# Performance work log

Hardware: AMD Instinct MI355X
Metric: run time of the kernel (lower is better)

The kernel has to match this reference:

```python
import jax, jax.numpy as jnp
import numpy as np

N, E, B = 100000, 1200000, 512
IN_DIM, HID, K, NCLS = 64, 64, 3, 10


def setup_inputs() -> dict:
    key = jax.random.key(0)
    ks = jax.random.split(key, 10)
    features = jax.random.normal(ks[0], (N, IN_DIM), jnp.float32)
    edge_src = jax.random.randint(ks[1], (E,), 0, N)
    edge_dst = jax.random.randint(ks[2], (E,), 0, N)
    graph_ids = jnp.sort(jax.random.randint(ks[3], (N,), 0, B))
    s1 = float(1.0 / np.sqrt(IN_DIM))
    W1 = jax.random.uniform(ks[4], (IN_DIM, HID), jnp.float32, -s1, s1)
    b1 = jnp.zeros((HID,), jnp.float32)
    s2 = float(1.0 / np.sqrt(HID))
    W2 = jax.random.uniform(ks[5], (HID, HID), jnp.float32, -s2, s2)
    b2 = jnp.zeros((HID,), jnp.float32)
    s3 = float(1.0 / np.sqrt(HID * 3))
    cw = jax.random.uniform(ks[6], (HID, HID, 3), jnp.float32, -s3, s3)
    cb = jax.random.uniform(ks[7], (HID,), jnp.float32, -s3, s3)
    Wc = jax.random.uniform(ks[8], (HID, NCLS), jnp.float32, -s2, s2)
    bc = jax.random.uniform(ks[9], (NCLS,), jnp.float32, -s2, s2)
    return dict(features=features, edge_src=edge_src, edge_dst=edge_dst,
                graph_ids=graph_ids, num_graphs=B,
                W1=W1, b1=b1, W2=W2, b2=b2, cw=cw, cb=cb, Wc=Wc, bc=bc)


def graph_conv(h, src, dst, W, b, n_nodes):
    # DGL GraphConv, norm='both', allow_zero_in_degree (degrees clamped to 1)
    ones = jnp.ones((src.shape[0],), h.dtype)
    out_deg = jnp.zeros((n_nodes,), h.dtype).at[src].add(ones)
    in_deg = jnp.zeros((n_nodes,), h.dtype).at[dst].add(ones)
    norm_s = jax.lax.rsqrt(jnp.clip(out_deg, 1.0, None))
    norm_d = jax.lax.rsqrt(jnp.clip(in_deg, 1.0, None))
    m = (h * norm_s[:, None]) @ W  # weight first; math identical to agg-first
    agg = jnp.zeros((n_nodes, W.shape[1]), h.dtype).at[dst].add(m[src])
    return agg * norm_d[:, None] + b


def sort_pool(h, gid, num_graphs, k):
    # DGL SortPooling: sort each node's features ascending along feature dim,
    # then take top-k nodes per graph by last feature value (descending),
    # zero-padding graphs with < k nodes. Output [num_graphs, k*D].
    hs = jnp.sort(h, axis=-1)
    key = hs[:, -1]
    order = jnp.lexsort((-key, gid))  # gid asc, key desc
    gid_s = gid[order]
    hs_s = hs[order]
    n = gid.shape[0]
    start = jnp.full((num_graphs,), n).at[gid_s].min(jnp.arange(n))
    rank = jnp.arange(n) - start[gid_s]  # within-graph rank by key desc
    mask = rank < k
    slot = gid_s * k + jnp.clip(rank, 0, k - 1)
    out = jnp.zeros((num_graphs * k, hs.shape[-1]), h.dtype).at[slot].add(
        jnp.where(mask[:, None], hs_s, jnp.zeros((), h.dtype)))
    return out.reshape(num_graphs, k * hs.shape[-1])


def reference(features, edge_src, edge_dst, graph_ids, num_graphs,
              W1, b1, W2, b2, cw, cb, Wc, bc):
    n = features.shape[0]
    h = jax.nn.relu(graph_conv(features, edge_src, edge_dst, W1, b1, n))
    h = jax.nn.relu(graph_conv(h, edge_src, edge_dst, W2, b2, n))
    p = sort_pool(h, graph_ids, num_graphs, K)          # [B, K*HID]
    x = p.reshape(num_graphs, HID, K)                    # faithful torch reshape
    # Conv1d(kernel=3, stride=1) on length-3 input -> length-1 output
    y = jax.nn.relu(jnp.einsum('bct,oct->bo', x, cw) + cb)
    return y @ Wc + bc
```

## Files before the change

kernel.cpp:

```cpp
#include <hip/hip_runtime.h>
#include <hip/hip_bf16.h>


#define PART 6272
#define HALFP (PART / 2)
#define MCH  64

__global__ void k_hist2(const int* __restrict__ esrc, const int* __restrict__ edst,
                        unsigned char* __restrict__ hd, unsigned char* __restrict__ hs,
                        int N, int E, int P) {
  __shared__ unsigned int ld[HALFP];
  __shared__ unsigned int ls[HALFP];
  const int b = blockIdx.x;
  const int p = b % P;
  const int m = b / P;
  const int base = p * PART;
  const int lim = min(PART, N - base);
  for (int i = threadIdx.x; i < HALFP; i += blockDim.x) { ld[i] = 0u; ls[i] = 0u; }
  __syncthreads();
  const long long cb = (long long)m * E / MCH;
  const long long ce = (long long)(m + 1) * E / MCH;
  const long long a0 = min((cb + 3) & ~3LL, ce);
  const long long nv = (ce - a0) >> 2;
  for (long long e = cb + threadIdx.x; e < a0; e += blockDim.x) {
    int d = edst[e] - base;
    if ((unsigned)d < (unsigned)lim) atomicAdd(&ld[d >> 1], 1u << ((d & 1) * 16));
    int s = esrc[e] - base;
    if ((unsigned)s < (unsigned)lim) atomicAdd(&ls[s >> 1], 1u << ((s & 1) * 16));
  }
  const int4* __restrict__ d4p = (const int4*)(edst + a0);
  const int4* __restrict__ s4p = (const int4*)(esrc + a0);
  for (long long i = threadIdx.x; i < nv; i += blockDim.x) {
    int4 d4 = d4p[i];
    int4 s4 = s4p[i];
    int d;
    d = d4.x - base; if ((unsigned)d < (unsigned)lim) atomicAdd(&ld[d >> 1], 1u << ((d & 1) * 16));
    d = d4.y - base; if ((unsigned)d < (unsigned)lim) atomicAdd(&ld[d >> 1], 1u << ((d & 1) * 16));
    d = d4.z - base; if ((unsigned)d < (unsigned)lim) atomicAdd(&ld[d >> 1], 1u << ((d & 1) * 16));
    d = d4.w - base; if ((unsigned)d < (unsigned)lim) atomicAdd(&ld[d >> 1], 1u << ((d & 1) * 16));
    d = s4.x - base; if ((unsigned)d < (unsigned)lim) atomicAdd(&ls[d >> 1], 1u << ((d & 1) * 16));
    d = s4.y - base; if ((unsigned)d < (unsigned)lim) atomicAdd(&ls[d >> 1], 1u << ((d & 1) * 16));
    d = s4.z - base; if ((unsigned)d < (unsigned)lim) atomicAdd(&ls[d >> 1], 1u << ((d & 1) * 16));
    d = s4.w - base; if ((unsigned)d < (unsigned)lim) atomicAdd(&ls[d >> 1], 1u << ((d & 1) * 16));
  }
  for (long long e = a0 + (nv << 2) + threadIdx.x; e < ce; e += blockDim.x) {
    int d = edst[e] - base;
    if ((unsigned)d < (unsigned)lim) atomicAdd(&ld[d >> 1], 1u << ((d & 1) * 16));
    int s = esrc[e] - base;
    if ((unsigned)s < (unsigned)lim) atomicAdd(&ls[s >> 1], 1u << ((s & 1) * 16));
  }
  __syncthreads();
  unsigned char* sd = hd + ((size_t)p * MCH + m) * PART;
  unsigned char* ss = hs + ((size_t)p * MCH + m) * PART;
  for (int i = threadIdx.x; i < lim; i += blockDim.x) {
    sd[i] = (unsigned char)((ld[i >> 1] >> ((i & 1) * 16)) & 0xffffu);
    ss[i] = (unsigned char)((ls[i >> 1] >> ((i & 1) * 16)) & 0xffffu);
  }
}

__global__ void k_off(unsigned char* __restrict__ hd, const unsigned char* __restrict__ hs,
                      int* __restrict__ deg_d, float* __restrict__ norm_s,
                      float* __restrict__ norm_d, int N, int P) {
  int v = blockIdx.x * blockDim.x + threadIdx.x;
  if (v >= N) return;
  int p = v / PART, loc = v % PART;
  size_t base = (size_t)p * MCH * PART + loc;
  int run = 0;
#pragma unroll
  for (int m = 0; m < MCH; ++m) {
    int t = hd[base + (size_t)m * PART];
    hd[base + (size_t)m * PART] = (unsigned char)run;
    run += t;
  }
  int s = 0;
#pragma unroll
  for (int m = 0; m < MCH; ++m) s += hs[base + (size_t)m * PART];
  deg_d[v] = run;
  norm_d[v] = rsqrtf((float)max(run, 1));
  norm_s[v] = rsqrtf((float)max(s, 1));
}

__global__ void k_scan1(const int* __restrict__ deg, int* __restrict__ rowptr,
                        int* __restrict__ bsum, int N) {
  __shared__ int sums[256];
  const int t = threadIdx.x;
  const int base = blockIdx.x * 2048 + t * 8;
  int loc[8];
  int tot = 0;
#pragma unroll
  for (int j = 0; j < 8; ++j) {
    int idx = base + j;
    loc[j] = tot;
    tot += (idx < N) ? deg[idx] : 0;
  }
  sums[t] = tot;
  __syncthreads();
  for (int off = 1; off < 256; off <<= 1) {
    int x = (t >= off) ? sums[t - off] : 0;
    __syncthreads();
    sums[t] += x;
    __syncthreads();
  }
  int excl = (t == 0) ? 0 : sums[t - 1];
#pragma unroll
  for (int j = 0; j < 8; ++j) {
    int idx = base + j;
    if (idx < N) rowptr[idx] = excl + loc[j];
  }
  if (t == 255) bsum[blockIdx.x] = sums[255];
}

__global__ void k_scan2(int* __restrict__ bsum, int nb) {
  int lane = threadIdx.x;
  int v = (lane < nb) ? bsum[lane] : 0;
  int inc = v;
#pragma unroll
  for (int off = 1; off < 64; off <<= 1) {
    int o = __shfl_up(inc, off, 64);
    if (lane >= off) inc += o;
  }
  if (lane < nb) bsum[lane] = inc - v;
}

__global__ void k_scan3(int* __restrict__ rowptr, const int* __restrict__ bsum, int N) {
  int v = blockIdx.x * blockDim.x + threadIdx.x;
  if (v < N) rowptr[v] += bsum[v >> 11];
}

__global__ void k_fill2(const int* __restrict__ esrc, const int* __restrict__ edst,
                        const unsigned char* __restrict__ hd, const int* __restrict__ rowptr,
                        int* __restrict__ csr, int N, int E, int P) {
  __shared__ int cur[PART];
  const int b = blockIdx.x;
  const int p = b % P;
  const int m = b / P;
  const int base = p * PART;
  const int lim = min(PART, N - base);
  const unsigned char* slice = hd + ((size_t)p * MCH + m) * PART;
  for (int i = threadIdx.x; i < lim; i += blockDim.x)
    cur[i] = rowptr[base + i] + (int)slice[i];
  __syncthreads();
  const long long cb = (long long)m * E / MCH;
  const long long ce = (long long)(m + 1) * E / MCH;
  const long long a0 = min((cb + 3) & ~3LL, ce);
  const long long nv = (ce - a0) >> 2;
  for (long long e = cb + threadIdx.x; e < a0; e += blockDim.x) {
    int d = edst[e] - base;
    if ((unsigned)d < (unsigned)lim) csr[atomicAdd(&cur[d], 1)] = esrc[e];
  }
  const int4* __restrict__ d4p = (const int4*)(edst + a0);
  const int4* __restrict__ s4p = (const int4*)(esrc + a0);
  for (long long i = threadIdx.x; i < nv; i += blockDim.x) {
    int4 d4 = d4p[i];
    int4 s4 = s4p[i];
    int d;
    d = d4.x - base; if ((unsigned)d < (unsigned)lim) csr[atomicAdd(&cur[d], 1)] = s4.x;
    d = d4.y - base; if ((unsigned)d < (unsigned)lim) csr[atomicAdd(&cur[d], 1)] = s4.y;
    d = d4.z - base; if ((unsigned)d < (unsigned)lim) csr[atomicAdd(&cur[d], 1)] = s4.z;
    d = d4.w - base; if ((unsigned)d < (unsigned)lim) csr[atomicAdd(&cur[d], 1)] = s4.w;
  }
  for (long long e = a0 + (nv << 2) + threadIdx.x; e < ce; e += blockDim.x) {
    int d = edst[e] - base;
    if ((unsigned)d < (unsigned)lim) csr[atomicAdd(&cur[d], 1)] = esrc[e];
  }
}

__global__ void __launch_bounds__(256) k_gemm64(
    const float* __restrict__ in, const float* __restrict__ norm,
    const float* __restrict__ W, float* __restrict__ out, int N) {
  __shared__ float Wl[4096];
  __shared__ float Ac[64 * 136];
  const int t = threadIdx.x;
  const int ch = (t & 7) * 8;
  const int nb = (t >> 3) * 4;
  for (int i = t; i < 1024; i += 256)
    ((float4*)Wl)[i] = ((const float4*)W)[i];

  const int NT = (N + 127) >> 7;
  for (int tile = blockIdx.x; tile < NT; tile += gridDim.x) {
    const int vbase = tile << 7;
    __syncthreads();
    for (int i = t; i < 2048; i += 256) {
      const int r = i >> 4;
      const int c = (i & 15) * 4;
      const int v = vbase + r;
      float4 val = make_float4(0.f, 0.f, 0.f, 0.f);
      if (v < N) val = *(const float4*)(in + (size_t)v * 64 + c);
      Ac[(c + 0) * 136 + r] = val.x;
      Ac[(c + 1) * 136 + r] = val.y;
      Ac[(c + 2) * 136 + r] = val.z;
      Ac[(c + 3) * 136 + r] = val.w;
    }
    __syncthreads();

    float acc[4][8];
#pragma unroll
    for (int j = 0; j < 4; ++j)
#pragma unroll
      for (int c = 0; c < 8; ++c) acc[j][c] = 0.f;

    for (int k = 0; k < 64; k += 4) {
#pragma unroll
      for (int kk = 0; kk < 4; ++kk) {
        const float4 aa = *(const float4*)&Ac[(k + kk) * 136 + nb];
        const float4 w0 = *(const float4*)&Wl[(k + kk) * 64 + ch];
        const float4 w1 = *(const float4*)&Wl[(k + kk) * 64 + ch + 4];
        const float an[4] = {aa.x, aa.y, aa.z, aa.w};
        const float wn[8] = {w0.x, w0.y, w0.z, w0.w, w1.x, w1.y, w1.z, w1.w};
#pragma unroll
        for (int j = 0; j < 4; ++j)
#pragma unroll
          for (int c = 0; c < 8; ++c)
            acc[j][c] = fmaf(an[j], wn[c], acc[j][c]);
      }
    }

#pragma unroll
    for (int j = 0; j < 4; ++j) {
      const int v = vbase + nb + j;
      if (v < N) {
        const float nm = norm[v];
        float4 o0, o1;
        o0.x = acc[j][0] * nm; o0.y = acc[j][1] * nm;
        o0.z = acc[j][2] * nm; o0.w = acc[j][3] * nm;
        o1.x = acc[j][4] * nm; o1.y = acc[j][5] * nm;
        o1.z = acc[j][6] * nm; o1.w = acc[j][7] * nm;
        *(float4*)(out + (size_t)v * 64 + ch)     = o0;
        *(float4*)(out + (size_t)v * 64 + ch + 4) = o1;
      }
    }
  }
}

__global__ void k_gather(const float* __restrict__ m, const int* __restrict__ rowptr,
                         const int* __restrict__ deg, const float* __restrict__ norm_d,
                         const float* __restrict__ bias, const int* __restrict__ csr,
                         float* __restrict__ h, float* __restrict__ key, int N) {
  const int w = blockIdx.x * (blockDim.x >> 6) + (threadIdx.x >> 6);
  if (w >= N) return;
  const int lane = threadIdx.x & 63;
  const int quad = lane & 15;
  const int grp = lane >> 4;
  const int start = rowptr[w];
  const int cnt = deg[w];
  float4 acc0 = make_float4(0.f, 0.f, 0.f, 0.f);
  float4 acc1 = make_float4(0.f, 0.f, 0.f, 0.f);
  int i = grp;
  for (; i + 4 < cnt; i += 8) {
    int s0 = csr[start + i];
    int s1 = csr[start + i + 4];
    const float4 v0 = *(const float4*)(m + (size_t)s0 * 64 + quad * 4);
    const float4 v1 = *(const float4*)(m + (size_t)s1 * 64 + quad * 4);
    acc0.x += v0.x; acc0.y += v0.y; acc0.z += v0.z; acc0.w += v0.w;
    acc1.x += v1.x; acc1.y += v1.y; acc1.z += v1.z; acc1.w += v1.w;
  }
  if (i < cnt) {
    int s0 = csr[start + i];
    const float4 v0 = *(const float4*)(m + (size_t)s0 * 64 + quad * 4);
    acc0.x += v0.x; acc0.y += v0.y; acc0.z += v0.z; acc0.w += v0.w;
  }
  acc0.x += acc1.x; acc0.y += acc1.y; acc0.z += acc1.z; acc0.w += acc1.w;
#pragma unroll
  for (int off = 16; off <= 32; off <<= 1) {
    acc0.x += __shfl_xor(acc0.x, off, 64);
    acc0.y += __shfl_xor(acc0.y, off, 64);
    acc0.z += __shfl_xor(acc0.z, off, 64);
    acc0.w += __shfl_xor(acc0.w, off, 64);
  }
  const float nd = norm_d[w];
  const float4 bq = *(const float4*)(bias + quad * 4);
  float4 o;
  o.x = fmaxf(fmaf(acc0.x, nd, bq.x), 0.f);
  o.y = fmaxf(fmaf(acc0.y, nd, bq.y), 0.f);
  o.z = fmaxf(fmaf(acc0.z, nd, bq.z), 0.f);
  o.w = fmaxf(fmaf(acc0.w, nd, bq.w), 0.f);
  if (grp == 0) *(float4*)(h + (size_t)w * 64 + quad * 4) = o;
  if (key != nullptr) {
    float mx = fmaxf(fmaxf(o.x, o.y), fmaxf(o.z, o.w));
#pragma unroll
    for (int off = 1; off < 16; off <<= 1) mx = fmaxf(mx, __shfl_xor(mx, off, 64));
    if (lane == 0) key[w] = mx;
  }
}

__global__ void k_bstart(const int* __restrict__ gid, int* __restrict__ gstart, int N) {
  int i = blockIdx.x * blockDim.x + threadIdx.x;
  if (i >= N) return;
  int g = gid[i];
  if (i == 0 || gid[i - 1] != g) gstart[g] = i;
}

__global__ void k_bfin(const int* __restrict__ gstart, int* __restrict__ gcnt,
                       int B, int N) {
  __shared__ int sm[512];
  const int g = threadIdx.x;
  sm[g] = (g < B) ? gstart[g] : 0x7fffffff;
  __syncthreads();
  for (int off = 1; off < 512; off <<= 1) {
    int x = (g + off < 512) ? sm[g + off] : 0x7fffffff;
    __syncthreads();
    sm[g] = min(sm[g], x);
    __syncthreads();
  }
  if (g < B) {
    int gs = gstart[g];
    int ns = (g + 1 < 512) ? min(sm[g + 1], N) : N;
    gcnt[g] = (gs < N) ? (ns - gs) : 0;
  }
}

__global__ void k_top3(const float* __restrict__ key, const int* __restrict__ gstart,
                       const int* __restrict__ gcnt, int* __restrict__ sel, int B) {
  const int lane = threadIdx.x & 63;
  const int g = blockIdx.x * (blockDim.x >> 6) + (threadIdx.x >> 6);
  if (g >= B) return;
  const int s = gstart[g], c = gcnt[g];
  float v0 = -1.f, v1 = -1.f, v2 = -1.f;
  int i0 = 0x7fffffff, i1 = 0x7fffffff, i2 = 0x7fffffff;
  for (int i = s + lane; i < s + c; i += 64) {
    float kv = key[i];
    if (kv > v0 || (kv == v0 && i < i0)) {
      v2 = v1; i2 = i1; v1 = v0; i1 = i0; v0 = kv; i0 = i;
    } else if (kv > v1 || (kv == v1 && i < i1)) {
      v2 = v1; i2 = i1; v1 = kv; i1 = i;
    } else if (kv > v2 || (kv == v2 && i < i2)) {
      v2 = kv; i2 = i;
    }
  }
  int ptr = 0;
  for (int r = 0; r < 3; ++r) {
    float mv = (ptr == 0) ? v0 : (ptr == 1) ? v1 : (ptr == 2) ? v2 : -1.f;
    int   mi = (ptr == 0) ? i0 : (ptr == 1) ? i1 : (ptr == 2) ? i2 : 0x7fffffff;
    float bv = mv; int bi = mi;
#pragma unroll
    for (int off = 32; off; off >>= 1) {
      float ov = __shfl_xor(bv, off, 64);
      int   oi = __shfl_xor(bi, off, 64);
      if (ov > bv || (ov == bv && oi < bi)) { bv = ov; bi = oi; }
    }
    if (bi == mi && ptr < 3) ptr++;
    if (lane == 0) sel[g * 3 + r] = (bi == 0x7fffffff) ? -1 : bi;
  }
}

__global__ void k_pool(const float* __restrict__ h, const int* __restrict__ sel,
                       float* __restrict__ p, int B) {
  const int lane = threadIdx.x & 63;
  const int w = blockIdx.x * (blockDim.x >> 6) + (threadIdx.x >> 6);
  if (w >= B * 3) return;
  int node = sel[w];
  float v = 0.f;
  if (node >= 0) {
    v = h[(size_t)node * 64 + lane];
    for (int k2 = 2; k2 <= 64; k2 <<= 1) {
      for (int j = k2 >> 1; j > 0; j >>= 1) {
        float o = __shfl_xor(v, j, 64);
        bool up = ((lane & k2) == 0);
        bool lower = ((lane & j) == 0);
        v = (lower == up) ? fminf(v, o) : fmaxf(v, o);
      }
    }
  }
  p[(size_t)w * 64 + lane] = v;
}

__global__ void k_cls(const float* __restrict__ p, const float* __restrict__ cw,
                      const float* __restrict__ cb, const float* __restrict__ Wc,
                      const float* __restrict__ bc, float* __restrict__ out, int B) {
  __shared__ float prow[192];
  const int b = blockIdx.x;
  const int lane = threadIdx.x;
  prow[lane] = p[(size_t)b * 192 + lane];
  prow[lane + 64] = p[(size_t)b * 192 + lane + 64];
  prow[lane + 128] = p[(size_t)b * 192 + lane + 128];
  __syncthreads();
  float y = cb[lane];
  for (int j = 0; j < 192; ++j) y = fmaf(prow[j], cw[lane * 192 + j], y);
  float ry = fmaxf(y, 0.f);
  for (int c = 0; c < 10; ++c) {
    float s = ry * Wc[lane * 10 + c];
#pragma unroll
    for (int off = 32; off; off >>= 1) s += __shfl_xor(s, off, 64);
    if (lane == 0) out[b * 10 + c] = s + bc[c];
  }
}

extern "C" void kernel_launch(void* const* d_in, const int* in_sizes, int n_in,
                              void* d_out, int out_size, void* d_ws, size_t ws_size,
                              hipStream_t stream) {
  const float* features = (const float*)d_in[0];
  const int*   esrc     = (const int*)d_in[1];
  const int*   edst     = (const int*)d_in[2];
  const int*   gid      = (const int*)d_in[3];
  const float* W1 = (const float*)d_in[5];
  const float* b1 = (const float*)d_in[6];
  const float* W2 = (const float*)d_in[7];
  const float* b2 = (const float*)d_in[8];
  const float* cw = (const float*)d_in[9];
  const float* cb = (const float*)d_in[10];
  const float* Wc = (const float*)d_in[11];
  const float* bc = (const float*)d_in[12];
  float* out = (float*)d_out;

  const int N = in_sizes[0] / 64;
  const int E = in_sizes[1];
  const int B = out_size / 10;
  const size_t N64 = (size_t)N * 64;
  const int nscan = (N + 2047) / 2048;
  const int P = (N + PART - 1) / PART;
  const size_t HSZ = (size_t)P * MCH * PART;
  const int NT = (N + 127) / 128;

  float* bufA   = (float*)d_ws;
  float* bufB   = bufA + N64;
  int*   deg_d  = (int*)(bufB + N64);
  float* norm_s = (float*)(deg_d + N);
  float* norm_d = norm_s + N;
  float* key    = norm_d + N;
  int*   rowptr = (int*)(key + N);
  int*   csr    = rowptr + N;
  int*   bsum   = csr + E;
  int*   gstart = bsum + 64;
  int*   gcnt   = gstart + B;
  int*   sel    = gcnt + B;
  float* p      = (float*)(sel + 3 * B);
  unsigned char* hd = (unsigned char*)(p + 192 * B);
  unsigned char* hs = hd + HSZ;

  const int TB = 256;

  k_hist2<<<P * MCH, TB, 0, stream>>>(esrc, edst, hd, hs, N, E, P);
  k_off<<<(N + TB - 1) / TB, TB, 0, stream>>>(hd, hs, deg_d, norm_s, norm_d, N, P);
  k_scan1<<<nscan, 256, 0, stream>>>(deg_d, rowptr, bsum, N);
  k_scan2<<<1, 64, 0, stream>>>(bsum, nscan);
  k_scan3<<<(N + TB - 1) / TB, TB, 0, stream>>>(rowptr, bsum, N);
  k_fill2<<<P * MCH, TB, 0, stream>>>(esrc, edst, hd, rowptr, csr, N, E, P);

  k_gemm64<<<NT, TB, 0, stream>>>(features, norm_s, W1, bufA, N);
  k_gather<<<(N + 3) / 4, TB, 0, stream>>>(bufA, rowptr, deg_d, norm_d, b1, csr,
                                           bufB, nullptr, N);

  k_gemm64<<<NT, TB, 0, stream>>>(bufB, norm_s, W2, bufA, N);
  k_gather<<<(N + 3) / 4, TB, 0, stream>>>(bufA, rowptr, deg_d, norm_d, b2, csr,
                                           bufB, key, N);

  hipMemsetAsync(gstart, 0x7f, (size_t)B * sizeof(int), stream);
  k_bstart<<<(N + TB - 1) / TB, TB, 0, stream>>>(gid, gstart, N);
  k_bfin<<<1, 512, 0, stream>>>(gstart, gcnt, B, N);
  k_top3<<<(B + 3) / 4, TB, 0, stream>>>(key, gstart, gcnt, sel, B);
  k_pool<<<(B * 3 + 3) / 4, TB, 0, stream>>>(bufB, sel, p, B);

  k_cls<<<B, 64, 0, stream>>>(p, cw, cb, Wc, bc, out, B);
}
```

Before: 322.9 us.

## Split histogram per array and pack fill cursors into byte counters

```diff
diff --git a/kernel.cpp b/kernel.cpp
--- a/kernel.cpp
+++ b/kernel.cpp
@@ -2,79 +2,71 @@
 #include <hip/hip_bf16.h>
 
 
-#define PART 6272
-#define HALFP (PART / 2)
+#define PART_H 25088
+#define HALF_H (PART_H / 2)
+#define PART_F 12544
+#define QUART_F (PART_F / 4)
 #define MCH  64
 
-__global__ void k_hist2(const int* __restrict__ esrc, const int* __restrict__ edst,
+__global__ void k_hist1(const int* __restrict__ esrc, const int* __restrict__ edst,
                         unsigned char* __restrict__ hd, unsigned char* __restrict__ hs,
-                        int N, int E, int P) {
-  __shared__ unsigned int ld[HALFP];
-  __shared__ unsigned int ls[HALFP];
+                        int N, int E, int PH) {
+  __shared__ unsigned int lc[HALF_H];
   const int b = blockIdx.x;
-  const int p = b % P;
-  const int m = b / P;
-  const int base = p * PART;
-  const int lim = min(PART, N - base);
-  for (int i = threadIdx.x; i < HALFP; i += blockDim.x) { ld[i] = 0u; ls[i] = 0u; }
+  const int half = PH * MCH;
+  const int a = b / half;
+  const int r = b % half;
+  const int p = r % PH;
+  const int m = r / PH;
+  const int* __restrict__ arr = a ? esrc : edst;
+  unsigned char* __restrict__ outp = a ? hs : hd;
+  const int base = p * PART_H;
+  const int lim = min(PART_H, N - base);
+  for (int i = threadIdx.x; i < HALF_H; i += blockDim.x) lc[i] = 0u;
   __syncthreads();
   const long long cb = (long long)m * E / MCH;
   const long long ce = (long long)(m + 1) * E / MCH;
   const long long a0 = min((cb + 3) & ~3LL, ce);
   const long long nv = (ce - a0) >> 2;
   for (long long e = cb + threadIdx.x; e < a0; e += blockDim.x) {
-    int d = edst[e] - base;
-    if ((unsigned)d < (unsigned)lim) atomicAdd(&ld[d >> 1], 1u << ((d & 1) * 16));
-    int s = esrc[e] - base;
-    if ((unsigned)s < (unsigned)lim) atomicAdd(&ls[s >> 1], 1u << ((s & 1) * 16));
-  }
-  const int4* __restrict__ d4p = (const int4*)(edst + a0);
-  const int4* __restrict__ s4p = (const int4*)(esrc + a0);
+    int d = arr[e] - base;
+    if ((unsigned)d < (unsigned)lim) atomicAdd(&lc[d >> 1], 1u << ((d & 1) * 16));
+  }
+  const int4* __restrict__ a4p = (const int4*)(arr + a0);
   for (long long i = threadIdx.x; i < nv; i += blockDim.x) {
-    int4 d4 = d4p[i];
-    int4 s4 = s4p[i];
+    int4 v4 = a4p[i];
     int d;
-    d = d4.x - base; if ((unsigned)d < (unsigned)lim) atomicAdd(&ld[d >> 1], 1u << ((d & 1) * 16));
-    d = d4.y - base; if ((unsigned)d < (unsigned)lim) atomicAdd(&ld[d >> 1], 1u << ((d & 1) * 16));
-    d = d4.z - base; if ((unsigned)d < (unsigned)lim) atomicAdd(&ld[d >> 1], 1u << ((d & 1) * 16));
-    d = d4.w - base; if ((unsigned)d < (unsigned)lim) atomicAdd(&ld[d >> 1], 1u << ((d & 1) * 16));
-    d = s4.x - base; if ((unsigned)d < (unsigned)lim) atomicAdd(&ls[d >> 1], 1u << ((d & 1) * 16));
-    d = s4.y - base; if ((unsigned)d < (unsigned)lim) atomicAdd(&ls[d >> 1], 1u << ((d & 1) * 16));
-    d = s4.z - base; if ((unsigned)d < (unsigned)lim) atomicAdd(&ls[d >> 1], 1u << ((d & 1) * 16));
-    d = s4.w - base; if ((unsigned)d < (unsigned)lim) atomicAdd(&ls[d >> 1], 1u << ((d & 1) * 16));
+    d = v4.x - base; if ((unsigned)d < (unsigned)lim) atomicAdd(&lc[d >> 1], 1u << ((d & 1) * 16));
+    d = v4.y - base; if ((unsigned)d < (unsigned)lim) atomicAdd(&lc[d >> 1], 1u << ((d & 1) * 16));
+    d = v4.z - base; if ((unsigned)d < (unsigned)lim) atomicAdd(&lc[d >> 1], 1u << ((d & 1) * 16));
+    d = v4.w - base; if ((unsigned)d < (unsigned)lim) atomicAdd(&lc[d >> 1], 1u << ((d & 1) * 16));
   }
   for (long long e = a0 + (nv << 2) + threadIdx.x; e < ce; e += blockDim.x) {
-    int d = edst[e] - base;
-    if ((unsigned)d < (unsigned)lim) atomicAdd(&ld[d >> 1], 1u << ((d & 1) * 16));
-    int s = esrc[e] - base;
-    if ((unsigned)s < (unsigned)lim) atomicAdd(&ls[s >> 1], 1u << ((s & 1) * 16));
-  }
-  __syncthreads();
-  unsigned char* sd = hd + ((size_t)p * MCH + m) * PART;
-  unsigned char* ss = hs + ((size_t)p * MCH + m) * PART;
-  for (int i = threadIdx.x; i < lim; i += blockDim.x) {
-    sd[i] = (unsigned char)((ld[i >> 1] >> ((i & 1) * 16)) & 0xffffu);
-    ss[i] = (unsigned char)((ls[i >> 1] >> ((i & 1) * 16)) & 0xffffu);
-  }
+    int d = arr[e] - base;
+    if ((unsigned)d < (unsigned)lim) atomicAdd(&lc[d >> 1], 1u << ((d & 1) * 16));
+  }
+  __syncthreads();
+  unsigned char* slice = outp + ((size_t)p * MCH + m) * PART_H;
+  for (int i = threadIdx.x; i < lim; i += blockDim.x)
+    slice[i] = (unsigned char)((lc[i >> 1] >> ((i & 1) * 16)) & 0xffffu);
 }
 
 __global__ void k_off(unsigned char* __restrict__ hd, const unsigned char* __restrict__ hs,
                       int* __restrict__ deg_d, float* __restrict__ norm_s,
-                      float* __restrict__ norm_d, int N, int P) {
+                      float* __restrict__ norm_d, int N) {
   int v = blockIdx.x * blockDim.x + threadIdx.x;
   if (v >= N) return;
-  int p = v / PART, loc = v % PART;
-  size_t base = (size_t)p * MCH * PART + loc;
+  size_t base = (size_t)(v / PART_H) * MCH * PART_H + (v % PART_H);
   int run = 0;
 #pragma unroll
   for (int m = 0; m < MCH; ++m) {
-    int t = hd[base + (size_t)m * PART];
-    hd[base + (size_t)m * PART] = (unsigned char)run;
+    int t = hd[base + (size_t)m * PART_H];
+    hd[base + (size_t)m * PART_H] = (unsigned char)run;
     run += t;
   }
   int s = 0;
 #pragma unroll
-  for (int m = 0; m < MCH; ++m) s += hs[base + (size_t)m * PART];
+  for (int m = 0; m < MCH; ++m) s += hs[base + (size_t)m * PART_H];
   deg_d[v] = run;
   norm_d[v] = rsqrtf((float)max(run, 1));
   norm_s[v] = rsqrtf((float)max(s, 1));
@@ -129,24 +121,30 @@
 
 __global__ void k_fill2(const int* __restrict__ esrc, const int* __restrict__ edst,
                         const unsigned char* __restrict__ hd, const int* __restrict__ rowptr,
-                        int* __restrict__ csr, int N, int E, int P) {
-  __shared__ int cur[PART];
+                        int* __restrict__ csr, int N, int E, int PF) {
+  __shared__ unsigned int cur4[QUART_F];
   const int b = blockIdx.x;
-  const int p = b % P;
-  const int m = b / P;
-  const int base = p * PART;
-  const int lim = min(PART, N - base);
-  const unsigned char* slice = hd + ((size_t)p * MCH + m) * PART;
-  for (int i = threadIdx.x; i < lim; i += blockDim.x)
-    cur[i] = rowptr[base + i] + (int)slice[i];
-  __syncthreads();
+  const int p = b % PF;
+  const int m = b / PF;
+  const int base = p * PART_F;
+  const int lim = min(PART_F, N - base);
+  const unsigned char* slice = hd + ((size_t)(p >> 1) * MCH + m) * PART_H
+                                  + (size_t)(p & 1) * PART_F;
+  const unsigned int* slice4 = (const unsigned int*)slice;
+  for (int i = threadIdx.x; i < QUART_F; i += blockDim.x) cur4[i] = slice4[i];
+  __syncthreads();
+  const int* __restrict__ rp = rowptr + base;
   const long long cb = (long long)m * E / MCH;
   const long long ce = (long long)(m + 1) * E / MCH;
   const long long a0 = min((cb + 3) & ~3LL, ce);
   const long long nv = (ce - a0) >> 2;
   for (long long e = cb + threadIdx.x; e < a0; e += blockDim.x) {
     int d = edst[e] - base;
-    if ((unsigned)d < (unsigned)lim) csr[atomicAdd(&cur[d], 1)] = esrc[e];
+    if ((unsigned)d < (unsigned)lim) {
+      unsigned int old = atomicAdd(&cur4[d >> 2], 1u << ((d & 3) * 8));
+      int off = (old >> ((d & 3) * 8)) & 0xff;
+      csr[rp[d] + off] = esrc[e];
+    }
   }
   const int4* __restrict__ d4p = (const int4*)(edst + a0);
   const int4* __restrict__ s4p = (const int4*)(esrc + a0);
@@ -154,14 +152,33 @@
     int4 d4 = d4p[i];
     int4 s4 = s4p[i];
     int d;
-    d = d4.x - base; if ((unsigned)d < (unsigned)lim) csr[atomicAdd(&cur[d], 1)] = s4.x;
-    d = d4.y - base; if ((unsigned)d < (unsigned)lim) csr[atomicAdd(&cur[d], 1)] = s4.y;
-    d = d4.z - base; if ((unsigned)d < (unsigned)lim) csr[atomicAdd(&cur[d], 1)] = s4.z;
-    d = d4.w - base; if ((unsigned)d < (unsigned)lim) csr[atomicAdd(&cur[d], 1)] = s4.w;
+    d = d4.x - base;
+    if ((unsigned)d < (unsigned)lim) {
+      unsigned int old = atomicAdd(&cur4[d >> 2], 1u << ((d & 3) * 8));
+      csr[rp[d] + ((old >> ((d & 3) * 8)) & 0xff)] = s4.x;
+    }
+    d = d4.y - base;
+    if ((unsigned)d < (unsigned)lim) {
+      unsigned int old = atomicAdd(&cur4[d >> 2], 1u << ((d & 3) * 8));
+      csr[rp[d] + ((old >> ((d & 3) * 8)) & 0xff)] = s4.y;
+    }
+    d = d4.z - base;
+    if ((unsigned)d < (unsigned)lim) {
+      unsigned int old = atomicAdd(&cur4[d >> 2], 1u << ((d & 3) * 8));
+      csr[rp[d] + ((old >> ((d & 3) * 8)) & 0xff)] = s4.z;
+    }
+    d = d4.w - base;
+    if ((unsigned)d < (unsigned)lim) {
+      unsigned int old = atomicAdd(&cur4[d >> 2], 1u << ((d & 3) * 8));
+      csr[rp[d] + ((old >> ((d & 3) * 8)) & 0xff)] = s4.w;
+    }
   }
   for (long long e = a0 + (nv << 2) + threadIdx.x; e < ce; e += blockDim.x) {
     int d = edst[e] - base;
-    if ((unsigned)d < (unsigned)lim) csr[atomicAdd(&cur[d], 1)] = esrc[e];
+    if ((unsigned)d < (unsigned)lim) {
+      unsigned int old = atomicAdd(&cur4[d >> 2], 1u << ((d & 3) * 8));
+      csr[rp[d] + ((old >> ((d & 3) * 8)) & 0xff)] = esrc[e];
+    }
   }
 }
 
@@ -407,8 +424,9 @@
   const int B = out_size / 10;
   const size_t N64 = (size_t)N * 64;
   const int nscan = (N + 2047) / 2048;
-  const int P = (N + PART - 1) / PART;
-  const size_t HSZ = (size_t)P * MCH * PART;
+  const int PH = (N + PART_H - 1) / PART_H;
+  const int PF = (N + PART_F - 1) / PART_F;
+  const size_t HSZ = (size_t)PH * MCH * PART_H;
   const int NT = (N + 127) / 128;
 
   float* bufA   = (float*)d_ws;
@@ -429,12 +447,12 @@
 
   const int TB = 256;
 
-  k_hist2<<<P * MCH, TB, 0, stream>>>(esrc, edst, hd, hs, N, E, P);
-  k_off<<<(N + TB - 1) / TB, TB, 0, stream>>>(hd, hs, deg_d, norm_s, norm_d, N, P);
+  k_hist1<<<2 * PH * MCH, TB, 0, stream>>>(esrc, edst, hd, hs, N, E, PH);
+  k_off<<<(N + TB - 1) / TB, TB, 0, stream>>>(hd, hs, deg_d, norm_s, norm_d, N);
   k_scan1<<<nscan, 256, 0, stream>>>(deg_d, rowptr, bsum, N);
   k_scan2<<<1, 64, 0, stream>>>(bsum, nscan);
   k_scan3<<<(N + TB - 1) / TB, TB, 0, stream>>>(rowptr, bsum, N);
-  k_fill2<<<P * MCH, TB, 0, stream>>>(esrc, edst, hd, rowptr, csr, N, E, P);
+  k_fill2<<<PF * MCH, TB, 0, stream>>>(esrc, edst, hd, rowptr, csr, N, E, PF);
 
   k_gemm64<<<NT, TB, 0, stream>>>(features, norm_s, W1, bufA, N);
   k_gather<<<(N + 3) / 4, TB, 0, stream>>>(bufA, rowptr, deg_d, norm_d, b1, csr,
```

Measured after the change: 328.2 us. About the same (+1.6%).
